# Kernel optimization log

Measured on AMD Instinct MI355X. Metric: run time of the kernel, lower is better.

The kernel has to match this reference:

```python
import jax, jax.numpy as jnp
import numpy as np

LEVEL_SIZES = [6, 24, 96, 384, 1536, 6144]
NUM_LABELS = sum(LEVEL_SIZES)  # 8190
IN_FEATURES = 768
BATCH = 8192


def setup_inputs() -> dict:
    key = jax.random.key(0)
    ks = jax.random.split(key, 2 * len(LEVEL_SIZES) + 1)
    inp = {"x": jax.random.normal(ks[0], (BATCH, IN_FEATURES), dtype=jnp.float32)}
    layer_in = IN_FEATURES
    for i, out in enumerate(LEVEL_SIZES):
        scale = 1.0 / np.sqrt(layer_in)
        inp[f"W{i}"] = jax.random.uniform(ks[2 * i + 1], (out, layer_in), jnp.float32, -scale, scale)
        inp[f"b{i}"] = jax.random.uniform(ks[2 * i + 2], (out,), jnp.float32, -scale, scale)
        layer_in += out
    # labels_by_level: a permutation of global label ids, split by level sizes
    rng = np.random.default_rng(42)
    inp["labels"] = jnp.asarray(rng.permutation(NUM_LABELS), dtype=jnp.int64)
    return inp


def reference(x, W0, b0, W1, b1, W2, b2, W3, b3, W4, b4, W5, b5, labels):
    Ws = [W0, W1, W2, W3, W4, W5]
    bs = [b0, b1, b2, b3, b4, b5]
    logits = jnp.zeros((x.shape[0], NUM_LABELS), dtype=x.dtype)
    cur = x
    off = 0
    for W, b, sz in zip(Ws, bs, LEVEL_SIZES):
        y = cur @ W.T + b  # [B, sz]
        lab = labels[off:off + sz]  # static slice: global columns for this level
        logits = logits.at[:, lab].set(y)
        cur = jax.nn.relu(jnp.concatenate([cur, y], axis=1))
        off += sz
    return logits
```

## Files before the change

### kernel.cpp

```cpp
#include <hip/hip_runtime.h>
#include <hip/hip_bf16.h>

#define BATCH 8192
#define NUM_LABELS 8190
#define CURW 2944
#define YW   8192

typedef __attribute__((ext_vector_type(4))) float f32x4;
typedef __attribute__((ext_vector_type(8))) short bf16x8;

#define VMCNT(n) asm volatile("s_waitcnt vmcnt(" #n ")" ::: "memory")
#define BAR() do { asm volatile("" ::: "memory"); __builtin_amdgcn_s_barrier(); asm volatile("" ::: "memory"); } while (0)
#define LGKM0() do { asm volatile("s_waitcnt lgkmcnt(0)" ::: "memory"); __builtin_amdgcn_sched_barrier(0); } while (0)

__device__ __forceinline__ unsigned short f2bf(float f) {
  unsigned u = __builtin_bit_cast(unsigned, f);
  unsigned r = u + 0x7fffu + ((u >> 16) & 1u);
  return (unsigned short)(r >> 16);
}
__device__ __forceinline__ float bf2f(unsigned short b) {
  return __builtin_bit_cast(float, (unsigned)b << 16);
}
__device__ __forceinline__ void gload_lds16(const void* g, void* l) {
  __builtin_amdgcn_global_load_lds(
      (const __attribute__((address_space(1))) void*)g,
      (__attribute__((address_space(3))) void*)l,
      16, 0, 0);
}

__global__ void k_convert_x(const float* __restrict__ x,
                            unsigned short* __restrict__ xraw,
                            unsigned short* __restrict__ cur) {
  int i = blockIdx.x * 256 + threadIdx.x;
  const int total = BATCH * 768 / 4;
  if (i >= total) return;
  float4 v = ((const float4*)x)[i];
  int e = i * 4;
  int row = e / 768;
  int col = e - row * 768;
  ushort4 a, c;
  a.x = f2bf(v.x); a.y = f2bf(v.y); a.z = f2bf(v.z); a.w = f2bf(v.w);
  c.x = f2bf(fmaxf(v.x, 0.f)); c.y = f2bf(fmaxf(v.y, 0.f));
  c.z = f2bf(fmaxf(v.z, 0.f)); c.w = f2bf(fmaxf(v.w, 0.f));
  *(ushort4*)(xraw + e) = a;
  *(ushort4*)(cur + (size_t)row * CURW + col) = c;
}

__global__ void k_zero_pads(unsigned short* __restrict__ cur) {
  const int PP = 130;
  int i = blockIdx.x * 256 + threadIdx.x;
  if (i >= BATCH * PP) return;
  int row = i / PP, p = i - row * PP;
  int col = p < 58 ? 774 + p : (p < 98 ? 856 + (p - 58) : 992 + (p - 98));
  cur[(size_t)row * CURW + col] = 0;
}

__device__ __forceinline__ int pad2real(int kp) {
  if (kp < 774)  return kp;
  if (kp < 832)  return -1;
  if (kp < 856)  return 774 + (kp - 832);
  if (kp < 896)  return -1;
  if (kp < 992)  return 798 + (kp - 896);
  if (kp < 1024) return -1;
  if (kp < 1408) return 894 + (kp - 1024);
  return 1278 + (kp - 1408);
}

__global__ void k_convert_w(const float* __restrict__ W, unsigned short* __restrict__ Wp,
                            int Nreal, int Kreal, int Kpad, int total) {
  int i = blockIdx.x * 256 + threadIdx.x;
  if (i >= total) return;
  int n = i / Kpad, kp = i - n * Kpad;
  int kr = pad2real(kp);
  float v = 0.f;
  if (n < Nreal && kr >= 0) v = W[(size_t)n * Kreal + kr];
  Wp[i] = f2bf(v);
}

__global__ void k_inv(const int* __restrict__ labels, int* __restrict__ inv) {
  int t = blockIdx.x * 256 + threadIdx.x;
  if (t < NUM_LABELS) inv[labels[t]] = t;
}

__global__ __launch_bounds__(256, 2) void k_fused_small(
    const unsigned short* __restrict__ xraw,
    const unsigned short* __restrict__ w0p,
    const unsigned short* __restrict__ w1p,
    const unsigned short* __restrict__ w2p,
    const float* __restrict__ b0, const float* __restrict__ b1,
    const float* __restrict__ b2,
    unsigned short* __restrict__ ybuf,
    unsigned short* __restrict__ cur) {
  __shared__ __align__(16) unsigned short As[32 * 1000];
  const int tid = threadIdx.x;
  const int l = tid & 63, w = tid >> 6;
  const int l15 = l & 15, q8 = (l >> 4) * 8;
  const int row0 = blockIdx.x * 32;
  const int mi = w >> 1;
  const int nj0 = w & 1;

  {
    const int r = tid >> 3, c8 = tid & 7;
    const unsigned short* src = xraw + (size_t)(row0 + r) * 768 + c8 * 96;
    unsigned short* dst = As + r * 1000 + c8 * 96;
#pragma unroll
    for (int i = 0; i < 12; ++i)
      *(bf16x8*)(dst + i * 8) = *(const bf16x8*)(src + i * 8);
    unsigned short* dz = As + r * 1000 + 768 + c8 * 28;
    ushort4 z = {0, 0, 0, 0};
#pragma unroll
    for (int i = 0; i < 7; ++i) *(ushort4*)(dz + i * 4) = z;
  }
  __syncthreads();

  auto level = [&](int K, int ntiles, int Nr, const unsigned short* W, int ldw,
                   const float* bias, int ycol, int ccol) {
    for (int n = nj0; n < ntiles; n += 2) {
      f32x4 acc = {0.f, 0.f, 0.f, 0.f};
      const unsigned short* wrow = W + (size_t)(n * 16 + l15) * ldw + q8;
      const unsigned short* arow = As + (mi * 16 + l15) * 1000 + q8;
#pragma unroll 2
      for (int k0 = 0; k0 < K; k0 += 32) {
        bf16x8 af = *(const bf16x8*)(arow + k0);
        bf16x8 bf = *(const bf16x8*)(wrow + k0);
        acc = __builtin_amdgcn_mfma_f32_16x16x32_bf16(af, bf, acc, 0, 0, 0);
      }
      int col = n * 16 + l15;
      if (col < Nr) {
        float bv = bias[col];
#pragma unroll
        for (int j = 0; j < 4; ++j) {
          int rl = mi * 16 + (l >> 4) * 4 + j;
          float y = acc[j] + bv;
          ybuf[(size_t)(row0 + rl) * YW + ycol + col] = f2bf(y);
          As[rl * 1000 + ccol + col] = f2bf(fmaxf(y, 0.f));
        }
      }
    }
    __syncthreads();
  };

  level(768, 1, 6,  w0p, 768, b0, 0,  768);

  {
    const int r = tid >> 3, c8 = tid & 7;
    unsigned short* p = As + r * 1000 + c8 * 96;
#pragma unroll
    for (int i = 0; i < 12; ++i) {
      bf16x8 v = *(bf16x8*)(p + i * 8);
#pragma unroll
      for (int j = 0; j < 8; ++j)
        if (((unsigned short)v[j]) & 0x8000u) v[j] = 0;
      *(bf16x8*)(p + i * 8) = v;
    }
  }
  __syncthreads();

  level(832, 2, 24, w1p, 832, b1, 6,  832);
  level(896, 6, 96, w2p, 896, b2, 30, 896);

  {
    const int r = tid >> 3, c8 = tid & 7;
    const unsigned short* srcl = As + r * 1000 + 768 + c8 * 28;
    unsigned short* dstg = cur + (size_t)(row0 + r) * CURW + 768 + c8 * 28;
#pragma unroll
    for (int i = 0; i < 7; ++i)
      *(ushort4*)(dstg + i * 4) = *(const ushort4*)(srcl + i * 4);
  }
}

__global__ __launch_bounds__(256, 2) void k_gemm(
    const unsigned short* __restrict__ A, int lda,
    const unsigned short* __restrict__ B, int ldb,
    const float* __restrict__ bias,
    unsigned short* __restrict__ ybuf,
    unsigned short* __restrict__ curout,
    int K, int Nreal, int yoff, int curoff) {
  __shared__ unsigned short Asmem[128 * 64];
  __shared__ unsigned short Bsmem[128 * 64];
  const int tid = threadIdx.x;
  const int lane = tid & 63;
  const int wid = tid >> 6;
  const int wr = wid >> 1, wc = wid & 1;
  const int brow = blockIdx.x * 128;
  const int bcol = blockIdx.y * 128;

  f32x4 acc[4][4] = {};

  for (int k0 = 0; k0 < K; k0 += 64) {
#pragma unroll
    for (int p = 0; p < 4; ++p) {
      int ch = wid * 4 + p;
      int eo = ch * 512 + lane * 8;
      int r = eo >> 6;
      int col = eo & 63;
      gload_lds16(A + (size_t)(brow + r) * lda + k0 + col, Asmem + ch * 512);
      gload_lds16(B + (size_t)(bcol + r) * ldb + k0 + col, Bsmem + ch * 512);
    }
    __syncthreads();
#pragma unroll
    for (int kk = 0; kk < 2; ++kk) {
      bf16x8 af[4], bfr[4];
      int colk = kk * 32 + (lane >> 4) * 8;
#pragma unroll
      for (int m = 0; m < 4; ++m)
        af[m] = *(const bf16x8*)(Asmem + (wr * 64 + m * 16 + (lane & 15)) * 64 + colk);
#pragma unroll
      for (int n = 0; n < 4; ++n)
        bfr[n] = *(const bf16x8*)(Bsmem + (wc * 64 + n * 16 + (lane & 15)) * 64 + colk);
#pragma unroll
      for (int m = 0; m < 4; ++m)
#pragma unroll
        for (int n = 0; n < 4; ++n)
          acc[m][n] = __builtin_amdgcn_mfma_f32_16x16x32_bf16(af[m], bfr[n], acc[m][n], 0, 0, 0);
    }
    __syncthreads();
  }

#pragma unroll
  for (int n = 0; n < 4; ++n) {
    int col = bcol + wc * 64 + n * 16 + (lane & 15);
    if (col >= Nreal) continue;
    float bv = bias[col];
#pragma unroll
    for (int m = 0; m < 4; ++m) {
#pragma unroll
      for (int j = 0; j < 4; ++j) {
        int row = brow + wr * 64 + m * 16 + (lane >> 4) * 4 + j;
        float y = acc[m][n][j] + bv;
        ybuf[(size_t)row * YW + yoff + col] = f2bf(y);
        if (curout) curout[(size_t)row * CURW + curoff + col] = f2bf(fmaxf(y, 0.f));
      }
    }
  }
}

__global__ __launch_bounds__(512, 2) void k_gemm256(
    const unsigned short* __restrict__ A, int lda,
    const unsigned short* __restrict__ B, int ldb,
    const float* __restrict__ bias,
    unsigned short* __restrict__ ybuf,
    unsigned short* __restrict__ curout,
    int K, int yoff, int curoff) {
  __shared__ __align__(16) unsigned short lds[65536];
  const int tid = threadIdx.x;
  const int l = tid & 63;
  const int w = tid >> 6;
  const int wr = w >> 2;
  const int wc = w & 3;
  const int l15 = l & 15;
  const int q8 = (l >> 4) * 8;
  const int sx = (l & 7) << 3;
  const int swz = ((l & 7) ^ (l >> 3)) * 8;

  const int bid = blockIdx.x;
  const int im = (bid & 7) * 4 + ((bid >> 3) & 3);
  const int in = bid >> 5;
  const int brow = im * 256, bcol = in * 256;

  const unsigned short* gA = A + (size_t)(brow + w * 8 + (l >> 3)) * lda + swz;
  const unsigned short* gB = B + (size_t)(bcol + w * 8 + (l >> 3)) * ldb + swz;

  unsigned short* const ldsp = lds;

  auto stageA = [&](int buf, int h, int kt) {
    const unsigned short* g = gA + (size_t)(h * 128) * lda + kt * 64;
    unsigned short* d = ldsp + buf * 16384 + h * 8192 + w * 512;
    gload_lds16(g, d);
    gload_lds16(g + (size_t)64 * lda, d + 4096);
  };
  auto stageB = [&](int buf, int h, int kt) {
    const unsigned short* g = gB + (size_t)(h * 128) * ldb + kt * 64;
    unsigned short* d = ldsp + 32768 + buf * 16384 + h * 8192 + w * 512;
    gload_lds16(g, d);
    gload_lds16(g + (size_t)64 * ldb, d + 4096);
  };

  const unsigned short* Arg[2] = { ldsp + wr * 8192, ldsp + 16384 + wr * 8192 };
  const unsigned short* Brg[2] = { ldsp + 32768 + (wc >> 1) * 8192, ldsp + 49152 + (wc >> 1) * 8192 };
  const int brB = (wc & 1) * 64;

  f32x4 acc[8][4] = {};
  bf16x8 aF[2][4], bF[2][4];

  auto ldA = [&](const unsigned short* R, int mhalf) {
#pragma unroll
    for (int kk = 0; kk < 2; ++kk)
#pragma unroll
      for (int m = 0; m < 4; ++m) {
        int r = mhalf * 64 + m * 16 + l15;
        int ck = kk * 32 + q8;
        aF[kk][m] = *(const bf16x8*)(R + r * 64 + (ck ^ sx));
      }
  };
  auto ldB = [&](const unsigned short* R, int nbase) {
#pragma unroll
    for (int kk = 0; kk < 2; ++kk)
#pragma unroll
      for (int n = 0; n < 2; ++n) {
        int r = brB + (nbase + n) * 16 + l15;
        int ck = kk * 32 + q8;
        bF[kk][nbase + n] = *(const bf16x8*)(R + r * 64 + (ck ^ sx));
      }
  };
  auto MMA = [&](int mbase, int nbase) {
    __builtin_amdgcn_s_setprio(1);
#pragma unroll
    for (int kk = 0; kk < 2; ++kk)
#pragma unroll
      for (int m = 0; m < 4; ++m)
#pragma unroll
        for (int n = 0; n < 2; ++n)
          acc[mbase + m][nbase + n] = __builtin_amdgcn_mfma_f32_16x16x32_bf16(
              aF[kk][m], bF[kk][nbase + n], acc[mbase + m][nbase + n], 0, 0, 0);
    __builtin_amdgcn_s_setprio(0);
  };

  const int KT = K >> 6;
  const int NT2 = KT >> 1;

  stageB(0, 0, 0); stageB(0, 1, 0); stageA(0, 0, 0); stageA(0, 1, 0);
  stageB(1, 0, 1); stageB(1, 1, 1); stageA(1, 0, 1);
  VMCNT(6);
  BAR();
  ldB(Brg[0], 0);

  for (int it = 0; it < NT2; ++it) {
    const bool more = (it + 1 < NT2);
    const int t1 = 2 * it + 1, t2 = 2 * it + 2, t3 = 2 * it + 3;
    ldA(Arg[0], 0); stageA(1, 1, t1);
    BAR(); LGKM0(); MMA(0, 0); BAR();
    ldB(Brg[0], 2);
    BAR(); LGKM0(); MMA(0, 2); BAR();
    ldA(Arg[0], 1);
    if (more) stageB(0, 0, t2);
    BAR(); LGKM0(); MMA(4, 0); BAR();
    if (more) { stageB(0, 1, t2); stageA(0, 0, t2); VMCNT(6); }
    else      { VMCNT(0); }
    BAR(); LGKM0(); MMA(4, 2); ldB(Brg[1], 0); BAR();
    ldA(Arg[1], 0);
    if (more) stageA(0, 1, t2);
    BAR(); LGKM0(); MMA(0, 0); BAR();
    ldB(Brg[1], 2);
    BAR(); LGKM0(); MMA(0, 2); BAR();
    ldA(Arg[1], 1);
    if (more) stageB(1, 0, t3);
    BAR(); LGKM0(); MMA(4, 0); BAR();
    if (more) { stageB(1, 1, t3); stageA(1, 0, t3); VMCNT(6); }
    BAR(); LGKM0(); MMA(4, 2);
    if (more) ldB(Brg[0], 0);
    BAR();
  }

  const int j4 = (l >> 4) * 4;
  float bv[4];
#pragma unroll
  for (int n = 0; n < 4; ++n) bv[n] = bias[bcol + wc * 64 + n * 16 + l15];
#pragma unroll
  for (int m = 0; m < 8; ++m) {
    int rowb = brow + wr * 128 + m * 16 + j4;
#pragma unroll
    for (int j = 0; j < 4; ++j) {
      size_t rbase = (size_t)(rowb + j);
#pragma unroll
      for (int n = 0; n < 4; ++n) {
        int col = bcol + wc * 64 + n * 16 + l15;
        float y = acc[m][n][j] + bv[n];
        ybuf[rbase * YW + yoff + col] = f2bf(y);
        if (curout) curout[rbase * CURW + curoff + col] = f2bf(fmaxf(y, 0.f));
      }
    }
  }
}

__global__ void k_gather(const unsigned short* __restrict__ ybuf,
                         const int* __restrict__ inv,
                         float* __restrict__ out) {
  const int half = NUM_LABELS / 2;
  int i = blockIdx.x * 256 + threadIdx.x;
  if (i >= BATCH * half) return;
  int row = i / half;
  int c2 = (i - row * half) * 2;
  int2 iv = *(const int2*)(inv + c2);
  const unsigned short* yr = ybuf + (size_t)row * YW;
  float2 v;
  v.x = bf2f(yr[iv.x]);
  v.y = bf2f(yr[iv.y]);
  *(float2*)(out + (size_t)row * NUM_LABELS + c2) = v;
}

extern "C" void kernel_launch(void* const* d_in, const int* in_sizes, int n_in,
                              void* d_out, int out_size, void* d_ws, size_t ws_size,
                              hipStream_t stream) {
  const float* x = (const float*)d_in[0];
  const float* W[6];
  const float* bias[6];
  for (int i = 0; i < 6; ++i) {
    W[i] = (const float*)d_in[1 + 2 * i];
    bias[i] = (const float*)d_in[2 + 2 * i];
  }
  const int* labels = (const int*)d_in[13];
  float* out = (float*)d_out;

  char* ws = (char*)d_ws;
  unsigned short* xraw = (unsigned short*)(ws);
  unsigned short* cur  = (unsigned short*)(ws + 12582912);
  unsigned short* wp   = (unsigned short*)(ws + 60817408);
  unsigned short* ybuf = (unsigned short*)(ws + 102744064);
  int* inv             = (int*)(ws + 236961792);

  static const int Kreal[6]  = {768, 774, 798, 894, 1278, 2814};
  static const int Kpad[6]   = {768, 832, 896, 1024, 1408, 2944};
  static const int Nreal[6]  = {6, 24, 96, 384, 1536, 6144};
  static const int Npad[6]   = {128, 128, 128, 384, 1536, 6144};
  static const size_t woff[6] = {0, 98304, 204800, 319488, 712704, 2875392};
  static const int yoff[6]   = {0, 6, 30, 126, 510, 2046};
  static const int curoff[6] = {768, 832, 896, 1024, 1408, 0};

  k_convert_x<<<BATCH * 768 / 4 / 256, 256, 0, stream>>>(x, xraw, cur);
  k_zero_pads<<<(BATCH * 130 + 255) / 256, 256, 0, stream>>>(cur);
  for (int i = 0; i < 6; ++i) {
    int tot = Npad[i] * Kpad[i];
    k_convert_w<<<(tot + 255) / 256, 256, 0, stream>>>(W[i], wp + woff[i], Nreal[i],
                                                       Kreal[i], Kpad[i], tot);
  }
  k_inv<<<(NUM_LABELS + 255) / 256, 256, 0, stream>>>(labels, inv);

  k_fused_small<<<BATCH / 32, 256, 0, stream>>>(
      xraw, wp + woff[0], wp + woff[1], wp + woff[2],
      bias[0], bias[1], bias[2], ybuf, cur);

  {
    dim3 grid(BATCH / 128, Npad[3] / 128);
    k_gemm<<<grid, 256, 0, stream>>>(cur, CURW, wp + woff[3], Kpad[3], bias[3], ybuf,
                                     cur, Kpad[3], Nreal[3], yoff[3], curoff[3]);
  }
  for (int i = 4; i < 6; ++i) {
    int nwg = (BATCH / 256) * (Npad[i] / 256);
    k_gemm256<<<nwg, 512, 0, stream>>>(cur, CURW, wp + woff[i], Kpad[i], bias[i], ybuf,
                                       (i < 5) ? cur : (unsigned short*)nullptr,
                                       Kpad[i], yoff[i], curoff[i]);
  }

  k_gather<<<(BATCH * (NUM_LABELS / 2) + 255) / 256, 256, 0, stream>>>(ybuf, inv, out);
}
```

Before: 635.7 us.

## Merge prep kernels, precompute GEMM addresses, and grid-stride the gather

Merges x conversion with pad zeroing, and merges the six weight conversions with the label inverse into one launch, cutting nine small launches to two. The gemm256 main loop now uses precomputed global and LDS fragment pointers with pointer increments instead of recomputing addresses inside lambdas. The gather kernel becomes a grid-stride loop over a fixed 8192-block grid with four elements per thread per pass. The weight kernel branches per element by level, and the gather loop adds 64-bit index arithmetic.

```diff
diff --git a/kernel.cpp b/kernel.cpp
--- a/kernel.cpp
+++ b/kernel.cpp
@@ -28,31 +28,31 @@
       16, 0, 0);
 }
 
-__global__ void k_convert_x(const float* __restrict__ x,
-                            unsigned short* __restrict__ xraw,
-                            unsigned short* __restrict__ cur) {
+__global__ void k_prep_x(const float* __restrict__ x,
+                         unsigned short* __restrict__ xraw,
+                         unsigned short* __restrict__ cur) {
+  const int TX = BATCH * 768 / 4;
   int i = blockIdx.x * 256 + threadIdx.x;
-  const int total = BATCH * 768 / 4;
-  if (i >= total) return;
-  float4 v = ((const float4*)x)[i];
-  int e = i * 4;
-  int row = e / 768;
-  int col = e - row * 768;
-  ushort4 a, c;
-  a.x = f2bf(v.x); a.y = f2bf(v.y); a.z = f2bf(v.z); a.w = f2bf(v.w);
-  c.x = f2bf(fmaxf(v.x, 0.f)); c.y = f2bf(fmaxf(v.y, 0.f));
-  c.z = f2bf(fmaxf(v.z, 0.f)); c.w = f2bf(fmaxf(v.w, 0.f));
-  *(ushort4*)(xraw + e) = a;
-  *(ushort4*)(cur + (size_t)row * CURW + col) = c;
-}
-
-__global__ void k_zero_pads(unsigned short* __restrict__ cur) {
+  if (i < TX) {
+    float4 v = ((const float4*)x)[i];
+    int e = i * 4;
+    int row = e / 768;
+    int col = e - row * 768;
+    ushort4 a, c;
+    a.x = f2bf(v.x); a.y = f2bf(v.y); a.z = f2bf(v.z); a.w = f2bf(v.w);
+    c.x = f2bf(fmaxf(v.x, 0.f)); c.y = f2bf(fmaxf(v.y, 0.f));
+    c.z = f2bf(fmaxf(v.z, 0.f)); c.w = f2bf(fmaxf(v.w, 0.f));
+    *(ushort4*)(xraw + e) = a;
+    *(ushort4*)(cur + (size_t)row * CURW + col) = c;
+    return;
+  }
+  int j = i - TX;
   const int PP = 130;
-  int i = blockIdx.x * 256 + threadIdx.x;
-  if (i >= BATCH * PP) return;
-  int row = i / PP, p = i - row * PP;
-  int col = p < 58 ? 774 + p : (p < 98 ? 856 + (p - 58) : 992 + (p - 98));
-  cur[(size_t)row * CURW + col] = 0;
+  if (j < BATCH * PP) {
+    int row = j / PP, p = j - row * PP;
+    int col = p < 58 ? 774 + p : (p < 98 ? 856 + (p - 58) : 992 + (p - 98));
+    cur[(size_t)row * CURW + col] = 0;
+  }
 }
 
 __device__ __forceinline__ int pad2real(int kp) {
@@ -66,20 +66,33 @@
   return 1278 + (kp - 1408);
 }
 
-__global__ void k_convert_w(const float* __restrict__ W, unsigned short* __restrict__ Wp,
-                            int Nreal, int Kreal, int Kpad, int total) {
-  int i = blockIdx.x * 256 + threadIdx.x;
-  if (i >= total) return;
-  int n = i / Kpad, kp = i - n * Kpad;
+template<int KPAD, int KREAL, int NREAL>
+__device__ __forceinline__ void convW(int rel, const float* __restrict__ W,
+                                      unsigned short* __restrict__ Wp) {
+  int n = rel / KPAD, kp = rel - n * KPAD;
   int kr = pad2real(kp);
   float v = 0.f;
-  if (n < Nreal && kr >= 0) v = W[(size_t)n * Kreal + kr];
-  Wp[i] = f2bf(v);
-}
-
-__global__ void k_inv(const int* __restrict__ labels, int* __restrict__ inv) {
-  int t = blockIdx.x * 256 + threadIdx.x;
-  if (t < NUM_LABELS) inv[labels[t]] = t;
+  if (n < NREAL && kr >= 0) v = W[(size_t)n * KREAL + kr];
+  Wp[rel] = f2bf(v);
+}
+
+__global__ void k_convert_w_all(const float* __restrict__ W0, const float* __restrict__ W1,
+                                const float* __restrict__ W2, const float* __restrict__ W3,
+                                const float* __restrict__ W4, const float* __restrict__ W5,
+                                const int* __restrict__ labels, int* __restrict__ inv,
+                                unsigned short* __restrict__ wp) {
+  int i = blockIdx.x * 256 + threadIdx.x;
+  if (i < NUM_LABELS) inv[labels[i]] = i;
+  if (i >= 20963328) return;
+  if (i < 319488) {
+    if (i < 98304)       convW<768, 768, 6>  (i,          W0, wp);
+    else if (i < 204800) convW<832, 774, 24> (i - 98304,  W1, wp + 98304);
+    else                 convW<896, 798, 96> (i - 204800, W2, wp + 204800);
+  } else {
+    if (i < 712704)       convW<1024, 894, 384>  (i - 319488,  W3, wp + 319488);
+    else if (i < 2875392) convW<1408, 1278, 1536>(i - 712704,  W4, wp + 712704);
+    else                  convW<2944, 2814, 6144>(i - 2875392, W5, wp + 2875392);
+  }
 }
 
 __global__ __launch_bounds__(256, 2) void k_fused_small(
@@ -258,50 +271,57 @@
   const int in = bid >> 5;
   const int brow = im * 256, bcol = in * 256;
 
-  const unsigned short* gA = A + (size_t)(brow + w * 8 + (l >> 3)) * lda + swz;
-  const unsigned short* gB = B + (size_t)(bcol + w * 8 + (l >> 3)) * ldb + swz;
-
-  unsigned short* const ldsp = lds;
-
-  auto stageA = [&](int buf, int h, int kt) {
-    const unsigned short* g = gA + (size_t)(h * 128) * lda + kt * 64;
-    unsigned short* d = ldsp + buf * 16384 + h * 8192 + w * 512;
-    gload_lds16(g, d);
-    gload_lds16(g + (size_t)64 * lda, d + 4096);
-  };
-  auto stageB = [&](int buf, int h, int kt) {
-    const unsigned short* g = gB + (size_t)(h * 128) * ldb + kt * 64;
-    unsigned short* d = ldsp + 32768 + buf * 16384 + h * 8192 + w * 512;
-    gload_lds16(g, d);
-    gload_lds16(g + (size_t)64 * ldb, d + 4096);
-  };
-
-  const unsigned short* Arg[2] = { ldsp + wr * 8192, ldsp + 16384 + wr * 8192 };
-  const unsigned short* Brg[2] = { ldsp + 32768 + (wc >> 1) * 8192, ldsp + 49152 + (wc >> 1) * 8192 };
+  const unsigned short* gAr0 = A + (size_t)(brow + w * 8 + (l >> 3)) * lda + swz;
+  const unsigned short* gAr1 = gAr0 + (size_t)64 * lda;
+  const unsigned short* gAr2 = gAr0 + (size_t)128 * lda;
+  const unsigned short* gAr3 = gAr0 + (size_t)192 * lda;
+  const unsigned short* gBr0 = B + (size_t)(bcol + w * 8 + (l >> 3)) * ldb + swz;
+  const unsigned short* gBr1 = gBr0 + (size_t)64 * ldb;
+  const unsigned short* gBr2 = gBr0 + (size_t)128 * ldb;
+  const unsigned short* gBr3 = gBr0 + (size_t)192 * ldb;
+
+  unsigned short* const dA00 = lds + w * 512;
+  unsigned short* const dA01 = lds + 8192 + w * 512;
+  unsigned short* const dA10 = lds + 16384 + w * 512;
+  unsigned short* const dA11 = lds + 24576 + w * 512;
+  unsigned short* const dB00 = lds + 32768 + w * 512;
+  unsigned short* const dB01 = lds + 40960 + w * 512;
+  unsigned short* const dB10 = lds + 49152 + w * 512;
+  unsigned short* const dB11 = lds + 57344 + w * 512;
+
+  const int cOff0 = (q8) ^ sx;
+  const int cOff1 = (32 + q8) ^ sx;
   const int brB = (wc & 1) * 64;
+  const unsigned short* const aB00 = lds + wr * 8192 + l15 * 64 + cOff0;
+  const unsigned short* const aB01 = lds + wr * 8192 + l15 * 64 + cOff1;
+  const unsigned short* const aB10 = lds + 16384 + wr * 8192 + l15 * 64 + cOff0;
+  const unsigned short* const aB11 = lds + 16384 + wr * 8192 + l15 * 64 + cOff1;
+  const unsigned short* const bB00 = lds + 32768 + (wc >> 1) * 8192 + (brB + l15) * 64 + cOff0;
+  const unsigned short* const bB01 = lds + 32768 + (wc >> 1) * 8192 + (brB + l15) * 64 + cOff1;
+  const unsigned short* const bB10 = lds + 49152 + (wc >> 1) * 8192 + (brB + l15) * 64 + cOff0;
+  const unsigned short* const bB11 = lds + 49152 + (wc >> 1) * 8192 + (brB + l15) * 64 + cOff1;
 
   f32x4 acc[8][4] = {};
   bf16x8 aF[2][4], bF[2][4];
 
-  auto ldA = [&](const unsigned short* R, int mhalf) {
-#pragma unroll
-    for (int kk = 0; kk < 2; ++kk)
-#pragma unroll
-      for (int m = 0; m < 4; ++m) {
-        int r = mhalf * 64 + m * 16 + l15;
-        int ck = kk * 32 + q8;
-        aF[kk][m] = *(const bf16x8*)(R + r * 64 + (ck ^ sx));
-      }
+  auto stage2 = [&](const unsigned short* glo, const unsigned short* ghi,
+                    unsigned short* dst, int koff) {
+    gload_lds16(glo + koff, dst);
+    gload_lds16(ghi + koff, dst + 4096);
   };
-  auto ldB = [&](const unsigned short* R, int nbase) {
-#pragma unroll
-    for (int kk = 0; kk < 2; ++kk)
-#pragma unroll
-      for (int n = 0; n < 2; ++n) {
-        int r = brB + (nbase + n) * 16 + l15;
-        int ck = kk * 32 + q8;
-        bF[kk][nbase + n] = *(const bf16x8*)(R + r * 64 + (ck ^ sx));
-      }
+  auto ldA = [&](const unsigned short* b0, const unsigned short* b1, int mhalf) {
+#pragma unroll
+    for (int m = 0; m < 4; ++m) {
+      aF[0][m] = *(const bf16x8*)(b0 + (mhalf * 64 + m * 16) * 64);
+      aF[1][m] = *(const bf16x8*)(b1 + (mhalf * 64 + m * 16) * 64);
+    }
+  };
+  auto ldB2 = [&](const unsigned short* b0, const unsigned short* b1, int nbase) {
+#pragma unroll
+    for (int n = 0; n < 2; ++n) {
+      bF[0][nbase + n] = *(const bf16x8*)(b0 + (nbase + n) * 16 * 64);
+      bF[1][nbase + n] = *(const bf16x8*)(b1 + (nbase + n) * 16 * 64);
+    }
   };
   auto MMA = [&](int mbase, int nbase) {
     __builtin_amdgcn_s_setprio(1);
@@ -319,37 +339,43 @@
   const int KT = K >> 6;
   const int NT2 = KT >> 1;
 
-  stageB(0, 0, 0); stageB(0, 1, 0); stageA(0, 0, 0); stageA(0, 1, 0);
-  stageB(1, 0, 1); stageB(1, 1, 1); stageA(1, 0, 1);
+  stage2(gBr0, gBr1, dB00, 0);
+  stage2(gBr2, gBr3, dB01, 0);
+  stage2(gAr0, gAr1, dA00, 0);
+  stage2(gAr2, gAr3, dA01, 0);
+  stage2(gBr0, gBr1, dB10, 64);
+  stage2(gBr2, gBr3, dB11, 64);
+  stage2(gAr0, gAr1, dA10, 64);
   VMCNT(6);
   BAR();
-  ldB(Brg[0], 0);
+  ldB2(bB00, bB01, 0);
 
   for (int it = 0; it < NT2; ++it) {
     const bool more = (it + 1 < NT2);
-    const int t1 = 2 * it + 1, t2 = 2 * it + 2, t3 = 2 * it + 3;
-    ldA(Arg[0], 0); stageA(1, 1, t1);
+    ldA(aB00, aB01, 0); stage2(gAr2, gAr3, dA11, 64);
     BAR(); LGKM0(); MMA(0, 0); BAR();
-    ldB(Brg[0], 2);
+    ldB2(bB00, bB01, 2);
     BAR(); LGKM0(); MMA(0, 2); BAR();
-    ldA(Arg[0], 1);
-    if (more) stageB(0, 0, t2);
+    ldA(aB00, aB01, 1);
+    if (more) stage2(gBr0, gBr1, dB00, 128);
     BAR(); LGKM0(); MMA(4, 0); BAR();
-    if (more) { stageB(0, 1, t2); stageA(0, 0, t2); VMCNT(6); }
+    if (more) { stage2(gBr2, gBr3, dB01, 128); stage2(gAr0, gAr1, dA00, 128); VMCNT(6); }
     else      { VMCNT(0); }
-    BAR(); LGKM0(); MMA(4, 2); ldB(Brg[1], 0); BAR();
-    ldA(Arg[1], 0);
-    if (more) stageA(0, 1, t2);
+    BAR(); LGKM0(); MMA(4, 2); ldB2(bB10, bB11, 0); BAR();
+    ldA(aB10, aB11, 0);
+    if (more) stage2(gAr2, gAr3, dA01, 128);
     BAR(); LGKM0(); MMA(0, 0); BAR();
-    ldB(Brg[1], 2);
+    ldB2(bB10, bB11, 2);
     BAR(); LGKM0(); MMA(0, 2); BAR();
-    ldA(Arg[1], 1);
-    if (more) stageB(1, 0, t3);
+    ldA(aB10, aB11, 1);
+    if (more) stage2(gBr0, gBr1, dB10, 192);
     BAR(); LGKM0(); MMA(4, 0); BAR();
-    if (more) { stageB(1, 1, t3); stageA(1, 0, t3); VMCNT(6); }
+    if (more) { stage2(gBr2, gBr3, dB11, 192); stage2(gAr0, gAr1, dA10, 192); VMCNT(6); }
     BAR(); LGKM0(); MMA(4, 2);
-    if (more) ldB(Brg[0], 0);
+    if (more) ldB2(bB00, bB01, 0);
     BAR();
+    gAr0 += 128; gAr1 += 128; gAr2 += 128; gAr3 += 128;
+    gBr0 += 128; gBr1 += 128; gBr2 += 128; gBr3 += 128;
   }
 
   const int j4 = (l >> 4) * 4;
@@ -377,16 +403,23 @@
                          const int* __restrict__ inv,
                          float* __restrict__ out) {
   const int half = NUM_LABELS / 2;
-  int i = blockIdx.x * 256 + threadIdx.x;
-  if (i >= BATCH * half) return;
-  int row = i / half;
-  int c2 = (i - row * half) * 2;
-  int2 iv = *(const int2*)(inv + c2);
-  const unsigned short* yr = ybuf + (size_t)row * YW;
-  float2 v;
-  v.x = bf2f(yr[iv.x]);
-  v.y = bf2f(yr[iv.y]);
-  *(float2*)(out + (size_t)row * NUM_LABELS + c2) = v;
+  const long total = (long)BATCH * half;
+  for (long b0 = (long)blockIdx.x * 1024; b0 < total; b0 += (long)gridDim.x * 1024) {
+    long i = b0 + threadIdx.x;
+#pragma unroll
+    for (int u = 0; u < 4; ++u, i += 256) {
+      if (i < total) {
+        int row = (int)(i / half);
+        int c2 = (int)(i - (long)row * half) * 2;
+        int2 iv = *(const int2*)(inv + c2);
+        const unsigned short* yr = ybuf + (size_t)row * YW;
+        float2 v;
+        v.x = bf2f(yr[iv.x]);
+        v.y = bf2f(yr[iv.y]);
+        *(float2*)(out + (size_t)row * NUM_LABELS + c2) = v;
+      }
+    }
+  }
 }
 
 extern "C" void kernel_launch(void* const* d_in, const int* in_sizes, int n_in,
@@ -409,7 +442,6 @@
   unsigned short* ybuf = (unsigned short*)(ws + 102744064);
   int* inv             = (int*)(ws + 236961792);
 
-  static const int Kreal[6]  = {768, 774, 798, 894, 1278, 2814};
   static const int Kpad[6]   = {768, 832, 896, 1024, 1408, 2944};
   static const int Nreal[6]  = {6, 24, 96, 384, 1536, 6144};
   static const int Npad[6]   = {128, 128, 128, 384, 1536, 6144};
@@ -417,14 +449,12 @@
   static const int yoff[6]   = {0, 6, 30, 126, 510, 2046};
   static const int curoff[6] = {768, 832, 896, 1024, 1408, 0};
 
-  k_convert_x<<<BATCH * 768 / 4 / 256, 256, 0, stream>>>(x, xraw, cur);
-  k_zero_pads<<<(BATCH * 130 + 255) / 256, 256, 0, stream>>>(cur);
-  for (int i = 0; i < 6; ++i) {
-    int tot = Npad[i] * Kpad[i];
-    k_convert_w<<<(tot + 255) / 256, 256, 0, stream>>>(W[i], wp + woff[i], Nreal[i],
-                                                       Kreal[i], Kpad[i], tot);
-  }
-  k_inv<<<(NUM_LABELS + 255) / 256, 256, 0, stream>>>(labels, inv);
+  {
+    int tot = BATCH * 768 / 4 + BATCH * 130;
+    k_prep_x<<<(tot + 255) / 256, 256, 0, stream>>>(x, xraw, cur);
+  }
+  k_convert_w_all<<<(20963328 + 255) / 256, 256, 0, stream>>>(
+      W[0], W[1], W[2], W[3], W[4], W[5], labels, inv, wp);
 
   k_fused_small<<<BATCH / 32, 256, 0, stream>>>(
       xraw, wp + woff[0], wp + woff[1], wp + woff[2],
@@ -442,5 +472,5 @@
                                        Kpad[i], yoff[i], curoff[i]);
   }
 
-  k_gather<<<(BATCH * (NUM_LABELS / 2) + 255) / 256, 256, 0, stream>>>(ybuf, inv, out);
-}
+  k_gather<<<8192, 256, 0, stream>>>(ybuf, inv, out);
+}
```

Result: no change. 648.1 us (+1.9%).
